# Kernel optimization log

Measured on AMD Instinct MI355X. Metric: run time of the kernel, lower is better.

## Reference

```python
import jax, jax.numpy as jnp
import numpy as np

D_MODEL = 512
NHEAD = 8
HEAD_DIM = D_MODEL // NHEAD
LN_EPS = 1e-5


def layer_norm(x, gamma, beta):
    mu = jnp.mean(x, axis=-1, keepdims=True)
    var = jnp.var(x, axis=-1, keepdims=True)
    return (x - mu) * jax.lax.rsqrt(var + LN_EPS) * gamma + beta


def setup_inputs() -> dict:
    key = jax.random.key(0)
    ks = jax.random.split(key, 10)
    B, L, S = 2, 4096, 4096
    d = D_MODEL
    s = 0.02
    return {
        "x": jax.random.normal(ks[0], (B, L, d), dtype=jnp.float32),
        "source": jax.random.normal(ks[1], (B, S, d), dtype=jnp.float32),
        "Wq": jax.random.normal(ks[2], (d, d), dtype=jnp.float32) * s,
        "Wk": jax.random.normal(ks[3], (d, d), dtype=jnp.float32) * s,
        "Wv": jax.random.normal(ks[4], (d, d), dtype=jnp.float32) * s,
        "Wm": jax.random.normal(ks[5], (d, d), dtype=jnp.float32) * s,
        "W1": jax.random.normal(ks[6], (2 * d, 2 * d), dtype=jnp.float32) * s,
        "W2": jax.random.normal(ks[7], (d, 2 * d), dtype=jnp.float32) * s,
        "g1": jnp.ones((d,), dtype=jnp.float32),
        "b1": jnp.zeros((d,), dtype=jnp.float32),
        "g2": jnp.ones((d,), dtype=jnp.float32),
        "b2": jnp.zeros((d,), dtype=jnp.float32),
    }


def reference(x, source, Wq, Wk, Wv, Wm, W1, W2, g1, b1, g2, b2):
    bs, L, _ = x.shape
    S = source.shape[1]
    # projections (torch Linear: y = x @ W^T), split into heads
    qw = (x @ Wq.T).reshape(bs, L, NHEAD, HEAD_DIM)
    kw = (source @ Wk.T).reshape(bs, S, NHEAD, HEAD_DIM)
    vw = (source @ Wv.T).reshape(bs, S, NHEAD, HEAD_DIM)
    # attention scores [B, L, S, H], softmax over S (axis=2)
    a = jnp.einsum('nlhd,nshd->nlsh', qw, kw) / jnp.sqrt(jnp.float32(HEAD_DIM))
    a = jax.nn.softmax(a, axis=2)
    o = jnp.einsum('nlsh,nshd->nlhd', a, vw).reshape(bs, L, NHEAD * HEAD_DIM)
    message = layer_norm(o @ Wm.T, g1, b1)
    h = jnp.concatenate([x, message], axis=2)  # [B, L, 2D]
    h = jax.nn.relu(h @ W1.T) @ W2.T
    message = layer_norm(h, g2, b2)
    return x + message
```

## Files before the change

kernel.cpp:

```cpp
#include <hip/hip_runtime.h>
#include <stdint.h>

typedef short bh8 __attribute__((ext_vector_type(8)));
typedef float fx4 __attribute__((ext_vector_type(4)));
typedef float fx16 __attribute__((ext_vector_type(16)));
typedef unsigned short u16;
typedef unsigned int u32;
typedef u32 u32x4 __attribute__((ext_vector_type(4)));
typedef u16 us4 __attribute__((ext_vector_type(4)));

#define NHEAD 8
#define HD 64
#define DM 512
#define SEQ 4096
#define ROWS 8192
#define CEXP 0.1803368801111244f

#define MODE_F32 0
#define MODE_BF16 1
#define MODE_RELU_BF16 2
#define MODE_KV 3

__device__ __forceinline__ u16 f2bf(float f) {
  union { float f; u32 u; } x; x.f = f;
  u32 u = x.u;
  u = u + 0x7fffu + ((u >> 16) & 1u);
  return (u16)(u >> 16);
}
__device__ __forceinline__ float bf2f(u16 h) {
  union { u32 u; float f; } x; x.u = ((u32)h) << 16;
  return x.f;
}
__device__ __forceinline__ void gll16(const void* g, void* l) {
  __builtin_amdgcn_global_load_lds(
      (const __attribute__((address_space(1))) void*)(uintptr_t)g,
      (__attribute__((address_space(3))) void*)(uintptr_t)l,
      16, 0, 0);
}
__device__ __forceinline__ fx4 mfma16(bh8 a, bh8 b, fx4 c) {
  return __builtin_amdgcn_mfma_f32_16x16x32_bf16(a, b, c, 0, 0, 0);
}
__device__ __forceinline__ fx16 mfma32(bh8 a, bh8 b, fx16 c) {
  return __builtin_amdgcn_mfma_f32_32x32x16_bf16(a, b, c, 0, 0, 0);
}
__device__ __forceinline__ u32 cvtpk(float lo, float hi) {
  u32 r; asm("v_cvt_pk_bf16_f32 %0, %1, %2" : "=v"(r) : "v"(lo), "v"(hi));
  return r;
}
__device__ __forceinline__ void pswap(u32& a, u32& b) {
  auto r = __builtin_amdgcn_permlane32_swap(a, b, false, false);
  a = r[0]; b = r[1];
}

__global__ __launch_bounds__(256) void cvt_all_kernel(
    const float* __restrict__ x, const float* __restrict__ src,
    const float* __restrict__ Wq, const float* __restrict__ Wk,
    const float* __restrict__ Wv, const float* __restrict__ Wm,
    const float* __restrict__ W1, const float* __restrict__ W2,
    u16* __restrict__ xb, u16* __restrict__ sb,
    u16* __restrict__ wqb, u16* __restrict__ wkvb, u16* __restrict__ wmb,
    u16* __restrict__ w1b, u16* __restrict__ w2b) {
  const int NQ = ROWS * DM / 4;
  const int TOT = 2 * NQ + 655360;
  for (int i = blockIdx.x * 256 + threadIdx.x; i < TOT; i += gridDim.x * 256) {
    const float* s; u16* d; int j;
    if (i < NQ)            { s = x;  d = xb;  j = i; }
    else if (i < 2 * NQ)   { s = src; d = sb; j = i - NQ; }
    else {
      int k = i - 2 * NQ;
      if (k < 65536)       { s = Wq; d = wqb;           j = k; }
      else if (k < 131072) { s = Wk; d = wkvb;          j = k - 65536; }
      else if (k < 196608) { s = Wv; d = wkvb + 262144; j = k - 131072; }
      else if (k < 262144) { s = Wm; d = wmb;           j = k - 196608; }
      else if (k < 524288) { s = W1; d = w1b;           j = k - 262144; }
      else                 { s = W2; d = w2b;           j = k - 524288; }
    }
    float4 v = ((const float4*)s)[j];
    us4 o; o.x = f2bf(v.x); o.y = f2bf(v.y); o.z = f2bf(v.z); o.w = f2bf(v.w);
    ((us4*)d)[j] = o;
  }
}

__device__ __forceinline__ void gemm_body(
    char* smem, const u16* __restrict__ A, const u16* __restrict__ Bw,
    void* __restrict__ Cp, void* __restrict__ C2p,
    int N, int K, int mode, float scl, int bx, int by) {
  char* sA = smem;
  char* sB = smem + 128 * 128;
  const int tid = threadIdx.x;
  const int w = tid >> 6, l = tid & 63;
  const int fr = l & 15, fg = l >> 4;
  const int row0 = by * 128, col0 = bx * 128;
  const int wr = (w >> 1) * 64, wc = (w & 1) * 64;

  fx4 acc[4][4];
#pragma unroll
  for (int m = 0; m < 4; m++)
#pragma unroll
    for (int n = 0; n < 4; n++)
#pragma unroll
      for (int r = 0; r < 4; r++) acc[m][n][r] = 0.f;

  for (int k0 = 0; k0 < K; k0 += 64) {
    __syncthreads();
#pragma unroll
    for (int i = 0; i < 4; i++) {
      int t = i * 256 + tid;
      int r = t >> 3, g = t & 7;
      int gs = g ^ (r & 7);
      gll16(A + (size_t)(row0 + r) * K + k0 + gs * 8, sA + i * 4096 + w * 1024);
      gll16(Bw + (size_t)(col0 + r) * K + k0 + gs * 8, sB + i * 4096 + w * 1024);
    }
    __syncthreads();
#pragma unroll
    for (int ks = 0; ks < 2; ks++) {
      bh8 af[4], bfr[4];
#pragma unroll
      for (int m = 0; m < 4; m++) {
        int rr = wr + m * 16 + fr;
        af[m] = *(const bh8*)(sA + rr * 128 + ((ks * 64 + fg * 16) ^ ((rr & 7) << 4)));
      }
#pragma unroll
      for (int n = 0; n < 4; n++) {
        int rr = wc + n * 16 + fr;
        bfr[n] = *(const bh8*)(sB + rr * 128 + ((ks * 64 + fg * 16) ^ ((rr & 7) << 4)));
      }
      __builtin_amdgcn_s_setprio(1);
#pragma unroll
      for (int m = 0; m < 4; m++)
#pragma unroll
        for (int n = 0; n < 4; n++) acc[m][n] = mfma16(af[m], bfr[n], acc[m][n]);
      __builtin_amdgcn_s_setprio(0);
    }
  }
#pragma unroll
  for (int m = 0; m < 4; m++)
#pragma unroll
    for (int n = 0; n < 4; n++)
#pragma unroll
      for (int r = 0; r < 4; r++) {
        int row = row0 + wr + m * 16 + fg * 4 + r;
        int col = col0 + wc + n * 16 + fr;
        float v = acc[m][n][r];
        if (mode == MODE_F32) {
          ((float*)Cp)[(size_t)row * N + col] = v;
        } else if (mode == MODE_BF16) {
          ((u16*)Cp)[(size_t)row * N + col] = f2bf(v * scl);
        } else if (mode == MODE_RELU_BF16) {
          ((u16*)Cp)[(size_t)row * N + col] = f2bf(v > 0.f ? v : 0.f);
        } else {
          int bb = row >> 12, s = row & 4095;
          if (col < 512) {
            int h = col >> 6, dd = col & 63;
            ((u16*)Cp)[(((size_t)((bb * 8 + h) * 8 + (dd >> 3))) * SEQ + s) * 8 + (dd & 7)] = f2bf(v);
          } else {
            int dd2 = col - 512;
            int h = dd2 >> 6, dd = dd2 & 63;
            ((u16*)C2p)[(((size_t)((bb * 8 + h) * 512 + (s >> 3))) * 64 + dd) * 8 + (s & 7)] = f2bf(v);
          }
        }
      }
}

__global__ __launch_bounds__(256) void qkv_kernel(
    const u16* __restrict__ xb, const u16* __restrict__ sb,
    const u16* __restrict__ wqb, const u16* __restrict__ wkvb,
    u16* __restrict__ Qb, u16* __restrict__ K2, u16* __restrict__ V2) {
  __shared__ __attribute__((aligned(16))) char smem[2 * 128 * 128];
  int bid = blockIdx.x;
  if (bid < 256) {
    gemm_body(smem, xb, wqb, Qb, nullptr, 512, 512, MODE_BF16, CEXP, bid & 3, bid >> 2);
  } else {
    int kb = bid - 256;
    gemm_body(smem, sb, wkvb, K2, V2, 1024, 512, MODE_KV, 1.0f, kb & 7, kb >> 3);
  }
}

__global__ __launch_bounds__(256) void gemm_bt_kernel(
    const u16* __restrict__ A, const u16* __restrict__ Bw,
    void* __restrict__ Cp, int N, int K, int mode) {
  __shared__ __attribute__((aligned(16))) char smem[2 * 128 * 128];
  gemm_body(smem, A, Bw, Cp, nullptr, N, K, mode, 1.0f, blockIdx.x, blockIdx.y);
}

__global__ __launch_bounds__(256) void gemm64_kernel(
    const u16* __restrict__ A, const u16* __restrict__ Bw,
    void* __restrict__ Cp, int M, int N, int K, int mode, float scl) {
  __shared__ __attribute__((aligned(16))) char smem[128 * 128 + 64 * 128];
  char* sA = smem;
  char* sB = smem + 128 * 128;
  const int tid = threadIdx.x;
  const int w = tid >> 6, l = tid & 63;
  const int fr = l & 15, fg = l >> 4;
  const int row0 = blockIdx.y * 128, col0 = blockIdx.x * 64;
  const int wr = (w >> 1) * 64, wc = (w & 1) * 32;

  fx4 acc[4][2];
#pragma unroll
  for (int m = 0; m < 4; m++)
#pragma unroll
    for (int n = 0; n < 2; n++)
#pragma unroll
      for (int r = 0; r < 4; r++) acc[m][n][r] = 0.f;

  for (int k0 = 0; k0 < K; k0 += 64) {
    __syncthreads();
#pragma unroll
    for (int i = 0; i < 4; i++) {
      int t = i * 256 + tid;
      int r = t >> 3, g = t & 7;
      int gs = g ^ (r & 7);
      gll16(A + (size_t)(row0 + r) * K + k0 + gs * 8, sA + i * 4096 + w * 1024);
    }
#pragma unroll
    for (int i = 0; i < 2; i++) {
      int t = i * 256 + tid;
      int r = t >> 3, g = t & 7;
      int gs = g ^ (r & 7);
      gll16(Bw + (size_t)(col0 + r) * K + k0 + gs * 8, sB + i * 4096 + w * 1024);
    }
    __syncthreads();
#pragma unroll
    for (int ks = 0; ks < 2; ks++) {
      bh8 af[4], bfr[2];
#pragma unroll
      for (int m = 0; m < 4; m++) {
        int rr = wr + m * 16 + fr;
        af[m] = *(const bh8*)(sA + rr * 128 + ((ks * 64 + fg * 16) ^ ((rr & 7) << 4)));
      }
#pragma unroll
      for (int n = 0; n < 2; n++) {
        int rr = wc + n * 16 + fr;
        bfr[n] = *(const bh8*)(sB + rr * 128 + ((ks * 64 + fg * 16) ^ ((rr & 7) << 4)));
      }
      __builtin_amdgcn_s_setprio(1);
#pragma unroll
      for (int m = 0; m < 4; m++)
#pragma unroll
        for (int n = 0; n < 2; n++) acc[m][n] = mfma16(af[m], bfr[n], acc[m][n]);
      __builtin_amdgcn_s_setprio(0);
    }
  }
#pragma unroll
  for (int m = 0; m < 4; m++)
#pragma unroll
    for (int n = 0; n < 2; n++)
#pragma unroll
      for (int r = 0; r < 4; r++) {
        int row = row0 + wr + m * 16 + fg * 4 + r;
        int col = col0 + wc + n * 16 + fr;
        float v = acc[m][n][r];
        if (mode == MODE_F32) ((float*)Cp)[(size_t)row * N + col] = v;
        else                  ((u16*)Cp)[(size_t)row * N + col] = f2bf(v * scl);
      }
}

__global__ __launch_bounds__(256, 3) void attn_kernel(
    const u16* __restrict__ Q, const u16* __restrict__ K2,
    const u16* __restrict__ V2,
    u16* __restrict__ Op0, u16* __restrict__ Op1,
    u16* __restrict__ Op2, u16* __restrict__ Op3,
    float* __restrict__ lsum, int ss) {
  const int tid = threadIdx.x;
  const int w = tid >> 6, l = tid & 63;
  const int l31 = l & 31, hi = l >> 5;

  int dl = blockIdx.x;
  int c = dl & 7, j = dl >> 3;
  int bh = 2 * c + (j >> (5 + ss));
  int rest = j & ((32 << ss) - 1);
  int qb = rest & 31, half = rest >> 5;
  const int b = bh >> 3, h = bh & 7;
  const int qr0 = b * SEQ + qb * 128 + w * 32;
  const int chunk = SEQ >> ss;
  const int sbase = half * chunk;
  const int NT = chunk / 64;

  bh8 qf[4];
#pragma unroll
  for (int ks = 0; ks < 4; ks++)
    qf[ks] = *(const bh8*)(Q + (size_t)(qr0 + l31) * DM + h * HD + ks * 16 + hi * 8);

  const u16* Kbase = K2 + (size_t)bh * 8 * SEQ * 8;
  const u16* Vbase = V2 + (size_t)bh * 512 * 64 * 8;

  fx16 o0, o1;
#pragma unroll
  for (int r = 0; r < 16; r++) { o0[r] = 0.f; o1[r] = 0.f; }
  float l_run = 0.f;

  for (int t = 0; t < NT; ++t) {
    const int s0 = sbase + t * 64;

    bh8 kf0[4], kf1[4];
#pragma unroll
    for (int ks = 0; ks < 4; ks++) {
      const u16* kp = Kbase + ((size_t)(ks * 2 + hi) * SEQ + s0 + l31) * 8;
      kf0[ks] = *(const bh8*)kp;
      kf1[ks] = *(const bh8*)(kp + 32 * 8);
    }

    fx16 s0v, s1v;
#pragma unroll
    for (int r = 0; r < 16; r++) { s0v[r] = 0.f; s1v[r] = 0.f; }
    __builtin_amdgcn_s_setprio(1);
#pragma unroll
    for (int ks = 0; ks < 4; ks++) {
      s0v = mfma32(kf0[ks], qf[ks], s0v);
      s1v = mfma32(kf1[ks], qf[ks], s1v);
    }
    __builtin_amdgcn_s_setprio(0);

    bh8 vf0[4], vf1[4];
#pragma unroll
    for (int ks = 0; ks < 4; ks++) {
      const u16* vp = Vbase + ((size_t)((s0 >> 3) + ks * 2 + hi) * 64 + l31) * 8;
      vf0[ks] = *(const bh8*)vp;
      vf1[ks] = *(const bh8*)(vp + 32 * 8);
    }

    float rs = 0.f;
#pragma unroll
    for (int r = 0; r < 16; r++) {
      s0v[r] = __builtin_amdgcn_exp2f(s0v[r]); rs += s0v[r];
    }
#pragma unroll
    for (int r = 0; r < 16; r++) {
      s1v[r] = __builtin_amdgcn_exp2f(s1v[r]); rs += s1v[r];
    }
    l_run += rs;

    __builtin_amdgcn_s_setprio(1);
#pragma unroll
    for (int ks = 0; ks < 4; ks++) {
      int o8 = (ks & 1) * 8;
      u32 w0a, w1a, w0b, w1b;
      if (ks < 2) {
        w0a = cvtpk(s0v[o8 + 0], s0v[o8 + 1]);
        w1a = cvtpk(s0v[o8 + 2], s0v[o8 + 3]);
        w0b = cvtpk(s0v[o8 + 4], s0v[o8 + 5]);
        w1b = cvtpk(s0v[o8 + 6], s0v[o8 + 7]);
      } else {
        w0a = cvtpk(s1v[o8 + 0], s1v[o8 + 1]);
        w1a = cvtpk(s1v[o8 + 2], s1v[o8 + 3]);
        w0b = cvtpk(s1v[o8 + 4], s1v[o8 + 5]);
        w1b = cvtpk(s1v[o8 + 6], s1v[o8 + 7]);
      }
      pswap(w0a, w0b); pswap(w1a, w1b);
      u32x4 fw; fw.x = w0a; fw.y = w1a; fw.z = w0b; fw.w = w1b;
      bh8 pa = __builtin_bit_cast(bh8, fw);
      o0 = mfma32(pa, vf0[ks], o0);
      o1 = mfma32(pa, vf1[ks], o1);
    }
    __builtin_amdgcn_s_setprio(0);
  }

  l_run += __shfl_xor(l_run, 32);
  if (hi == 0)
    lsum[half * 65536 + bh * 4096 + ((qr0 & 4095) + l31)] = l_run;
  u16* Op = (half == 0) ? Op0 : (half == 1) ? Op1 : (half == 2) ? Op2 : Op3;
#pragma unroll
  for (int r = 0; r < 16; r++) {
    int crow = (r & 3) + 8 * (r >> 2) + 4 * hi;
    size_t row = (size_t)(qr0 + crow);
    Op[row * DM + h * HD + l31] = f2bf(o0[r]);
    Op[row * DM + h * HD + 32 + l31] = f2bf(o1[r]);
  }
}

__global__ __launch_bounds__(256) void merge_kernel(
    const u16* __restrict__ Oa, const u16* __restrict__ Ob,
    const u16* __restrict__ Oc, const u16* __restrict__ Od,
    const float* __restrict__ lsum, u16* __restrict__ out, int split) {
  int i8 = blockIdx.x * 256 + threadIdx.x;
  size_t base = (size_t)i8 * 8;
  if (base >= (size_t)ROWS * DM) return;
  int row = (int)(base >> 9), col = (int)(base & 511);
  int h = col >> 6, b = row >> 12, lr = row & 4095;
  int li = (b * 8 + h) * 4096 + lr;
  float acc[8];
#pragma unroll
  for (int j = 0; j < 8; j++) acc[j] = 0.f;
  float lt = 0.f;
  const u16* ops[4] = {Oa, Ob, Oc, Od};
  for (int s = 0; s < split; s++) {
    lt += lsum[s * 65536 + li];
    bh8 v = *(const bh8*)(ops[s] + base);
#pragma unroll
    for (int j = 0; j < 8; j++) acc[j] += bf2f((u16)v[j]);
  }
  float inv = 1.f / lt;
  bh8 o;
#pragma unroll
  for (int j = 0; j < 8; j++) o[j] = (short)f2bf(acc[j] * inv);
  *(bh8*)(out + base) = o;
}

__global__ __launch_bounds__(256) void ln_concat_kernel(
    const u16* __restrict__ M0, const u16* __restrict__ xb,
    const float* __restrict__ g1, const float* __restrict__ b1,
    u16* __restrict__ h) {
  const int row = blockIdx.x;
  const int tid = threadIdx.x;
  const u16* mr = M0 + (size_t)row * 512;
  float v0 = bf2f(mr[tid]), v1 = bf2f(mr[tid + 256]);
  float s = v0 + v1, s2 = v0 * v0 + v1 * v1;
#pragma unroll
  for (int off = 1; off <= 32; off <<= 1) {
    s += __shfl_xor(s, off);
    s2 += __shfl_xor(s2, off);
  }
  __shared__ float red[8];
  const int w = tid >> 6, l = tid & 63;
  if (l == 0) { red[w] = s; red[w + 4] = s2; }
  __syncthreads();
  s = red[0] + red[1] + red[2] + red[3];
  s2 = red[4] + red[5] + red[6] + red[7];
  float mu = s * (1.f / 512.f);
  float var = s2 * (1.f / 512.f) - mu * mu;
  float rstd = rsqrtf(var + 1e-5f);
  u16* hr = h + (size_t)row * 1024;
  const u16* xrow = xb + (size_t)row * 512;
  for (int e = tid; e < 512; e += 256) {
    hr[e] = xrow[e];
    hr[512 + e] = f2bf((bf2f(mr[e]) - mu) * rstd * g1[e] + b1[e]);
  }
}

__global__ __launch_bounds__(256) void ln_res_kernel(
    const float* __restrict__ F, const float* __restrict__ X,
    const float* __restrict__ g2, const float* __restrict__ b2,
    float* __restrict__ out) {
  const int row = blockIdx.x;
  const int tid = threadIdx.x;
  const float* fr_ = F + (size_t)row * 512;
  float v0 = fr_[tid], v1 = fr_[tid + 256];
  float s = v0 + v1, s2 = v0 * v0 + v1 * v1;
#pragma unroll
  for (int off = 1; off <= 32; off <<= 1) {
    s += __shfl_xor(s, off);
    s2 += __shfl_xor(s2, off);
  }
  __shared__ float red[8];
  const int w = tid >> 6, l = tid & 63;
  if (l == 0) { red[w] = s; red[w + 4] = s2; }
  __syncthreads();
  s = red[0] + red[1] + red[2] + red[3];
  s2 = red[4] + red[5] + red[6] + red[7];
  float mu = s * (1.f / 512.f);
  float var = s2 * (1.f / 512.f) - mu * mu;
  float rstd = rsqrtf(var + 1e-5f);
  const float* xr = X + (size_t)row * 512;
  float* orow = out + (size_t)row * 512;
  for (int e = tid; e < 512; e += 256)
    orow[e] = xr[e] + (fr_[e] - mu) * rstd * g2[e] + b2[e];
}

extern "C" void kernel_launch(void* const* d_in, const int* in_sizes, int n_in,
                              void* d_out, int out_size, void* d_ws, size_t ws_size,
                              hipStream_t stream) {
  (void)in_sizes; (void)n_in; (void)out_size;
  const float* x   = (const float*)d_in[0];
  const float* src = (const float*)d_in[1];
  const float* Wq  = (const float*)d_in[2];
  const float* Wk  = (const float*)d_in[3];
  const float* Wv  = (const float*)d_in[4];
  const float* Wm  = (const float*)d_in[5];
  const float* W1  = (const float*)d_in[6];
  const float* W2  = (const float*)d_in[7];
  const float* g1  = (const float*)d_in[8];
  const float* b1  = (const float*)d_in[9];
  const float* g2  = (const float*)d_in[10];
  const float* b2  = (const float*)d_in[11];

  char* ws = (char*)d_ws;
  u16* xb   = (u16*)(ws + 0);
  u16* sb   = (u16*)(ws + 8388608);
  u16* wqb  = (u16*)(ws + 16777216);
  u16* wkvb = (u16*)(ws + 17301504);
  u16* wmb  = (u16*)(ws + 18350080);
  u16* w1b  = (u16*)(ws + 18874368);
  u16* w2b  = (u16*)(ws + 20971520);
  u16* Qb   = (u16*)(ws + 22020096);
  u16* K2b  = (u16*)(ws + 30408704);
  u16* V2b  = (u16*)(ws + 38797312);
  u16* Op0  = (u16*)(ws + 47185920);
  u16* Op1  = (u16*)(ws + 8388608);

  const bool big = ws_size >= 73400320u;
  int ss = big ? 2 : 1;
  u16* Op2; u16* Op3; float* lsum;
  if (big) {
    Op2  = (u16*)(ws + 55574528);
    Op3  = (u16*)(ws + 63963136);
    lsum = (float*)(ws + 72351744);
  } else {
    Op2  = Op0; Op3 = Op0;
    lsum = (float*)(ws + 55574528);
  }
  u16* Obf  = (u16*)(ws + 22020096);
  u16* M0b  = (u16*)(ws + 30408704);
  u16* hb   = (u16*)(ws + 38797312);
  u16* h1b  = (u16*)(ws + 22020096);
  float* fb = (float*)(ws + 38797312);

  cvt_all_kernel<<<2048, 256, 0, stream>>>(x, src, Wq, Wk, Wv, Wm, W1, W2,
                                           xb, sb, wqb, wkvb, wmb, w1b, w2b);
  qkv_kernel<<<768, 256, 0, stream>>>(xb, sb, wqb, wkvb, Qb, K2b, V2b);
  attn_kernel<<<512 << ss, 256, 0, stream>>>(Qb, K2b, V2b, Op0, Op1, Op2, Op3, lsum, ss);
  merge_kernel<<<2048, 256, 0, stream>>>(Op0, Op1, Op2, Op3, lsum, Obf, 1 << ss);
  gemm64_kernel<<<dim3(8, 64), 256, 0, stream>>>(Obf, wmb, M0b, ROWS, 512, 512, MODE_BF16, 1.0f);
  ln_concat_kernel<<<8192, 256, 0, stream>>>(M0b, xb, g1, b1, hb);
  gemm_bt_kernel<<<dim3(8, 64), 256, 0, stream>>>(hb, w1b, h1b, 1024, 1024, MODE_RELU_BF16);
  gemm64_kernel<<<dim3(8, 64), 256, 0, stream>>>(h1b, w2b, fb, ROWS, 512, 1024, MODE_F32, 1.0f);
  ln_res_kernel<<<8192, 256, 0, stream>>>(fb, x, g2, b2, (float*)d_out);
}
```

Baseline: 224.6 us.

## Pre-swizzle weights into MFMA fragment order and load B directly to registers

Weights are converted into an MFMA-fragment-ordered layout during the bf16 conversion pass, so the GEMM core loads B fragments straight from global memory into registers and no longer stages B through LDS. The FFN1 GEMM reads its A operand from two separate sources (x and the normalized message), which removes the concat copy in the layernorm kernel. The FFN2 output is now stored as bf16 instead of f32, halving its write and read traffic at some cost in precision. The trade-off is uncoalesced-looking direct global B loads that depend on cache hits, plus halved LDS use.

```diff
diff --git a/kernel.cpp b/kernel.cpp
--- a/kernel.cpp
+++ b/kernel.cpp
@@ -16,7 +16,6 @@
 #define ROWS 8192
 #define CEXP 0.1803368801111244f
 
-#define MODE_F32 0
 #define MODE_BF16 1
 #define MODE_RELU_BF16 2
 #define MODE_KV 3
@@ -50,6 +49,11 @@
 __device__ __forceinline__ void pswap(u32& a, u32& b) {
   auto r = __builtin_amdgcn_permlane32_swap(a, b, false, false);
   a = r[0]; b = r[1];
+}
+
+__device__ __forceinline__ int fragidx4(int n, int k4, int K) {
+  return (((((n >> 4) * (K >> 5) + (k4 >> 5)) << 2) + ((k4 >> 3) & 3)) * 16 + (n & 15)) * 2
+         + ((k4 & 7) >> 2);
 }
 
 __global__ __launch_bounds__(256) void cvt_all_kernel(
@@ -63,88 +67,93 @@
   const int NQ = ROWS * DM / 4;
   const int TOT = 2 * NQ + 655360;
   for (int i = blockIdx.x * 256 + threadIdx.x; i < TOT; i += gridDim.x * 256) {
-    const float* s; u16* d; int j;
+    const float* s; u16* d; int j; int widx = -1;
     if (i < NQ)            { s = x;  d = xb;  j = i; }
     else if (i < 2 * NQ)   { s = src; d = sb; j = i - NQ; }
     else {
       int k = i - 2 * NQ;
-      if (k < 65536)       { s = Wq; d = wqb;           j = k; }
-      else if (k < 131072) { s = Wk; d = wkvb;          j = k - 65536; }
-      else if (k < 196608) { s = Wv; d = wkvb + 262144; j = k - 131072; }
-      else if (k < 262144) { s = Wm; d = wmb;           j = k - 196608; }
-      else if (k < 524288) { s = W1; d = w1b;           j = k - 262144; }
-      else                 { s = W2; d = w2b;           j = k - 524288; }
+      int n, k4, K;
+      if (k < 65536)       { s = Wq; d = wqb; j = k;          n = j >> 7; k4 = (j & 127) << 2; K = 512; }
+      else if (k < 131072) { s = Wk; d = wkvb; j = k - 65536; n = j >> 7; k4 = (j & 127) << 2; K = 512; }
+      else if (k < 196608) { s = Wv; d = wkvb; j = k - 131072; n = (j >> 7) + 512; k4 = (j & 127) << 2; K = 512; }
+      else if (k < 262144) { s = Wm; d = wmb; j = k - 196608; n = j >> 7; k4 = (j & 127) << 2; K = 512; }
+      else if (k < 524288) { s = W1; d = w1b; j = k - 262144; n = j >> 8; k4 = (j & 255) << 2; K = 1024; }
+      else                 { s = W2; d = w2b; j = k - 524288; n = j >> 8; k4 = (j & 255) << 2; K = 1024; }
+      widx = fragidx4(n, k4, K);
     }
     float4 v = ((const float4*)s)[j];
     us4 o; o.x = f2bf(v.x); o.y = f2bf(v.y); o.z = f2bf(v.z); o.w = f2bf(v.w);
-    ((us4*)d)[j] = o;
-  }
-}
-
-__device__ __forceinline__ void gemm_body(
-    char* smem, const u16* __restrict__ A, const u16* __restrict__ Bw,
-    void* __restrict__ Cp, void* __restrict__ C2p,
+    ((us4*)d)[widx < 0 ? j : widx] = o;
+  }
+}
+
+template <int NTW>
+__device__ __forceinline__ void gemm_core(
+    char* sA, const u16* __restrict__ A, const u16* __restrict__ A2, int strideA,
+    const u16* __restrict__ Bw, void* __restrict__ Cp, void* __restrict__ C2p,
     int N, int K, int mode, float scl, int bx, int by) {
-  char* sA = smem;
-  char* sB = smem + 128 * 128;
   const int tid = threadIdx.x;
   const int w = tid >> 6, l = tid & 63;
   const int fr = l & 15, fg = l >> 4;
-  const int row0 = by * 128, col0 = bx * 128;
-  const int wr = (w >> 1) * 64, wc = (w & 1) * 64;
-
-  fx4 acc[4][4];
+  const int row0 = by * 128, col0 = bx * NTW * 32;
+  const int wr = (w >> 1) * 64, wc = (w & 1) * NTW * 16;
+
+  fx4 acc[4][NTW];
 #pragma unroll
   for (int m = 0; m < 4; m++)
 #pragma unroll
-    for (int n = 0; n < 4; n++)
+    for (int n = 0; n < NTW; n++)
 #pragma unroll
       for (int r = 0; r < 4; r++) acc[m][n][r] = 0.f;
 
   for (int k0 = 0; k0 < K; k0 += 64) {
+    const u16* Asrc = (k0 < 512) ? A : A2;
+    const int kk = k0 & (strideA - 1);
     __syncthreads();
 #pragma unroll
     for (int i = 0; i < 4; i++) {
       int t = i * 256 + tid;
       int r = t >> 3, g = t & 7;
       int gs = g ^ (r & 7);
-      gll16(A + (size_t)(row0 + r) * K + k0 + gs * 8, sA + i * 4096 + w * 1024);
-      gll16(Bw + (size_t)(col0 + r) * K + k0 + gs * 8, sB + i * 4096 + w * 1024);
-    }
+      gll16(Asrc + (size_t)(row0 + r) * strideA + kk + gs * 8, sA + i * 4096 + w * 1024);
+    }
+    bh8 bfr[2][NTW];
+#pragma unroll
+    for (int ks = 0; ks < 2; ks++)
+#pragma unroll
+      for (int n = 0; n < NTW; n++) {
+        const u16* bp = Bw +
+            ((((size_t)((col0 + wc) >> 4) + n) * (K >> 5) + (k0 >> 5) + ks) * 4 + fg) * 128 +
+            fr * 8;
+        bfr[ks][n] = *(const bh8*)bp;
+      }
     __syncthreads();
 #pragma unroll
     for (int ks = 0; ks < 2; ks++) {
-      bh8 af[4], bfr[4];
+      bh8 af[4];
 #pragma unroll
       for (int m = 0; m < 4; m++) {
         int rr = wr + m * 16 + fr;
         af[m] = *(const bh8*)(sA + rr * 128 + ((ks * 64 + fg * 16) ^ ((rr & 7) << 4)));
       }
-#pragma unroll
-      for (int n = 0; n < 4; n++) {
-        int rr = wc + n * 16 + fr;
-        bfr[n] = *(const bh8*)(sB + rr * 128 + ((ks * 64 + fg * 16) ^ ((rr & 7) << 4)));
-      }
       __builtin_amdgcn_s_setprio(1);
 #pragma unroll
       for (int m = 0; m < 4; m++)
 #pragma unroll
-        for (int n = 0; n < 4; n++) acc[m][n] = mfma16(af[m], bfr[n], acc[m][n]);
+        for (int n = 0; n < NTW; n++) acc[m][n] = mfma16(af[m], bfr[ks][n], acc[m][n]);
       __builtin_amdgcn_s_setprio(0);
     }
   }
 #pragma unroll
   for (int m = 0; m < 4; m++)
 #pragma unroll
-    for (int n = 0; n < 4; n++)
+    for (int n = 0; n < NTW; n++)
 #pragma unroll
       for (int r = 0; r < 4; r++) {
         int row = row0 + wr + m * 16 + fg * 4 + r;
         int col = col0 + wc + n * 16 + fr;
         float v = acc[m][n][r];
-        if (mode == MODE_F32) {
-          ((float*)Cp)[(size_t)row * N + col] = v;
-        } else if (mode == MODE_BF16) {
+        if (mode == MODE_BF16) {
           ((u16*)Cp)[(size_t)row * N + col] = f2bf(v * scl);
         } else if (mode == MODE_RELU_BF16) {
           ((u16*)Cp)[(size_t)row * N + col] = f2bf(v > 0.f ? v : 0.f);
@@ -166,93 +175,32 @@
     const u16* __restrict__ xb, const u16* __restrict__ sb,
     const u16* __restrict__ wqb, const u16* __restrict__ wkvb,
     u16* __restrict__ Qb, u16* __restrict__ K2, u16* __restrict__ V2) {
-  __shared__ __attribute__((aligned(16))) char smem[2 * 128 * 128];
+  __shared__ __attribute__((aligned(16))) char smem[128 * 128];
   int bid = blockIdx.x;
   if (bid < 256) {
-    gemm_body(smem, xb, wqb, Qb, nullptr, 512, 512, MODE_BF16, CEXP, bid & 3, bid >> 2);
+    gemm_core<4>(smem, xb, xb, 512, wqb, Qb, nullptr, 512, 512, MODE_BF16, CEXP,
+                 bid & 3, bid >> 2);
   } else {
     int kb = bid - 256;
-    gemm_body(smem, sb, wkvb, K2, V2, 1024, 512, MODE_KV, 1.0f, kb & 7, kb >> 3);
-  }
-}
-
-__global__ __launch_bounds__(256) void gemm_bt_kernel(
-    const u16* __restrict__ A, const u16* __restrict__ Bw,
-    void* __restrict__ Cp, int N, int K, int mode) {
-  __shared__ __attribute__((aligned(16))) char smem[2 * 128 * 128];
-  gemm_body(smem, A, Bw, Cp, nullptr, N, K, mode, 1.0f, blockIdx.x, blockIdx.y);
+    gemm_core<4>(smem, sb, sb, 512, wkvb, K2, V2, 1024, 512, MODE_KV, 1.0f,
+                 kb & 7, kb >> 3);
+  }
+}
+
+__global__ __launch_bounds__(256) void ffn1_kernel(
+    const u16* __restrict__ xb, const u16* __restrict__ m0ln,
+    const u16* __restrict__ w1b, u16* __restrict__ h1) {
+  __shared__ __attribute__((aligned(16))) char smem[128 * 128];
+  gemm_core<4>(smem, xb, m0ln, 512, w1b, h1, nullptr, 1024, 1024, MODE_RELU_BF16, 1.0f,
+               blockIdx.x, blockIdx.y);
 }
 
 __global__ __launch_bounds__(256) void gemm64_kernel(
-    const u16* __restrict__ A, const u16* __restrict__ Bw,
-    void* __restrict__ Cp, int M, int N, int K, int mode, float scl) {
-  __shared__ __attribute__((aligned(16))) char smem[128 * 128 + 64 * 128];
-  char* sA = smem;
-  char* sB = smem + 128 * 128;
-  const int tid = threadIdx.x;
-  const int w = tid >> 6, l = tid & 63;
-  const int fr = l & 15, fg = l >> 4;
-  const int row0 = blockIdx.y * 128, col0 = blockIdx.x * 64;
-  const int wr = (w >> 1) * 64, wc = (w & 1) * 32;
-
-  fx4 acc[4][2];
-#pragma unroll
-  for (int m = 0; m < 4; m++)
-#pragma unroll
-    for (int n = 0; n < 2; n++)
-#pragma unroll
-      for (int r = 0; r < 4; r++) acc[m][n][r] = 0.f;
-
-  for (int k0 = 0; k0 < K; k0 += 64) {
-    __syncthreads();
-#pragma unroll
-    for (int i = 0; i < 4; i++) {
-      int t = i * 256 + tid;
-      int r = t >> 3, g = t & 7;
-      int gs = g ^ (r & 7);
-      gll16(A + (size_t)(row0 + r) * K + k0 + gs * 8, sA + i * 4096 + w * 1024);
-    }
-#pragma unroll
-    for (int i = 0; i < 2; i++) {
-      int t = i * 256 + tid;
-      int r = t >> 3, g = t & 7;
-      int gs = g ^ (r & 7);
-      gll16(Bw + (size_t)(col0 + r) * K + k0 + gs * 8, sB + i * 4096 + w * 1024);
-    }
-    __syncthreads();
-#pragma unroll
-    for (int ks = 0; ks < 2; ks++) {
-      bh8 af[4], bfr[2];
-#pragma unroll
-      for (int m = 0; m < 4; m++) {
-        int rr = wr + m * 16 + fr;
-        af[m] = *(const bh8*)(sA + rr * 128 + ((ks * 64 + fg * 16) ^ ((rr & 7) << 4)));
-      }
-#pragma unroll
-      for (int n = 0; n < 2; n++) {
-        int rr = wc + n * 16 + fr;
-        bfr[n] = *(const bh8*)(sB + rr * 128 + ((ks * 64 + fg * 16) ^ ((rr & 7) << 4)));
-      }
-      __builtin_amdgcn_s_setprio(1);
-#pragma unroll
-      for (int m = 0; m < 4; m++)
-#pragma unroll
-        for (int n = 0; n < 2; n++) acc[m][n] = mfma16(af[m], bfr[n], acc[m][n]);
-      __builtin_amdgcn_s_setprio(0);
-    }
-  }
-#pragma unroll
-  for (int m = 0; m < 4; m++)
-#pragma unroll
-    for (int n = 0; n < 2; n++)
-#pragma unroll
-      for (int r = 0; r < 4; r++) {
-        int row = row0 + wr + m * 16 + fg * 4 + r;
-        int col = col0 + wc + n * 16 + fr;
-        float v = acc[m][n][r];
-        if (mode == MODE_F32) ((float*)Cp)[(size_t)row * N + col] = v;
-        else                  ((u16*)Cp)[(size_t)row * N + col] = f2bf(v * scl);
-      }
+    const u16* __restrict__ A, const u16* __restrict__ A2, int strideA,
+    const u16* __restrict__ Bw, u16* __restrict__ Cp, int K, float scl) {
+  __shared__ __attribute__((aligned(16))) char smem[128 * 128];
+  gemm_core<2>(smem, A, A2, strideA, Bw, Cp, nullptr, 512, K, MODE_BF16, scl,
+               blockIdx.x, blockIdx.y);
 }
 
 __global__ __launch_bounds__(256, 3) void attn_kernel(
@@ -396,10 +344,9 @@
   *(bh8*)(out + base) = o;
 }
 
-__global__ __launch_bounds__(256) void ln_concat_kernel(
-    const u16* __restrict__ M0, const u16* __restrict__ xb,
-    const float* __restrict__ g1, const float* __restrict__ b1,
-    u16* __restrict__ h) {
+__global__ __launch_bounds__(256) void ln_kernel(
+    const u16* __restrict__ M0, const float* __restrict__ g1,
+    const float* __restrict__ b1, u16* __restrict__ out) {
   const int row = blockIdx.x;
   const int tid = threadIdx.x;
   const u16* mr = M0 + (size_t)row * 512;
@@ -419,22 +366,19 @@
   float mu = s * (1.f / 512.f);
   float var = s2 * (1.f / 512.f) - mu * mu;
   float rstd = rsqrtf(var + 1e-5f);
-  u16* hr = h + (size_t)row * 1024;
-  const u16* xrow = xb + (size_t)row * 512;
-  for (int e = tid; e < 512; e += 256) {
-    hr[e] = xrow[e];
-    hr[512 + e] = f2bf((bf2f(mr[e]) - mu) * rstd * g1[e] + b1[e]);
-  }
+  u16* orow = out + (size_t)row * 512;
+  for (int e = tid; e < 512; e += 256)
+    orow[e] = f2bf((bf2f(mr[e]) - mu) * rstd * g1[e] + b1[e]);
 }
 
 __global__ __launch_bounds__(256) void ln_res_kernel(
-    const float* __restrict__ F, const float* __restrict__ X,
+    const u16* __restrict__ F, const float* __restrict__ X,
     const float* __restrict__ g2, const float* __restrict__ b2,
     float* __restrict__ out) {
   const int row = blockIdx.x;
   const int tid = threadIdx.x;
-  const float* fr_ = F + (size_t)row * 512;
-  float v0 = fr_[tid], v1 = fr_[tid + 256];
+  const u16* fr_ = F + (size_t)row * 512;
+  float v0 = bf2f(fr_[tid]), v1 = bf2f(fr_[tid + 256]);
   float s = v0 + v1, s2 = v0 * v0 + v1 * v1;
 #pragma unroll
   for (int off = 1; off <= 32; off <<= 1) {
@@ -453,7 +397,7 @@
   const float* xr = X + (size_t)row * 512;
   float* orow = out + (size_t)row * 512;
   for (int e = tid; e < 512; e += 256)
-    orow[e] = xr[e] + (fr_[e] - mu) * rstd * g2[e] + b2[e];
+    orow[e] = xr[e] + (bf2f(fr_[e]) - mu) * rstd * g2[e] + b2[e];
 }
 
 extern "C" void kernel_launch(void* const* d_in, const int* in_sizes, int n_in,
@@ -500,18 +444,18 @@
   }
   u16* Obf  = (u16*)(ws + 22020096);
   u16* M0b  = (u16*)(ws + 30408704);
-  u16* hb   = (u16*)(ws + 38797312);
+  u16* m0ln = (u16*)(ws + 38797312);
   u16* h1b  = (u16*)(ws + 22020096);
-  float* fb = (float*)(ws + 38797312);
+  u16* fb   = (u16*)(ws + 47185920);
 
   cvt_all_kernel<<<2048, 256, 0, stream>>>(x, src, Wq, Wk, Wv, Wm, W1, W2,
                                            xb, sb, wqb, wkvb, wmb, w1b, w2b);
   qkv_kernel<<<768, 256, 0, stream>>>(xb, sb, wqb, wkvb, Qb, K2b, V2b);
   attn_kernel<<<512 << ss, 256, 0, stream>>>(Qb, K2b, V2b, Op0, Op1, Op2, Op3, lsum, ss);
   merge_kernel<<<2048, 256, 0, stream>>>(Op0, Op1, Op2, Op3, lsum, Obf, 1 << ss);
-  gemm64_kernel<<<dim3(8, 64), 256, 0, stream>>>(Obf, wmb, M0b, ROWS, 512, 512, MODE_BF16, 1.0f);
-  ln_concat_kernel<<<8192, 256, 0, stream>>>(M0b, xb, g1, b1, hb);
-  gemm_bt_kernel<<<dim3(8, 64), 256, 0, stream>>>(hb, w1b, h1b, 1024, 1024, MODE_RELU_BF16);
-  gemm64_kernel<<<dim3(8, 64), 256, 0, stream>>>(h1b, w2b, fb, ROWS, 512, 1024, MODE_F32, 1.0f);
+  gemm64_kernel<<<dim3(8, 64), 256, 0, stream>>>(Obf, Obf, 512, wmb, M0b, 512, 1.0f);
+  ln_kernel<<<8192, 256, 0, stream>>>(M0b, g1, b1, m0ln);
+  ffn1_kernel<<<dim3(8, 64), 256, 0, stream>>>(xb, m0ln, w1b, h1b);
+  gemm64_kernel<<<dim3(8, 64), 256, 0, stream>>>(h1b, h1b, 1024, w2b, fb, 1024, 1.0f);
   ln_res_kernel<<<8192, 256, 0, stream>>>(fb, x, g2, b2, (float*)d_out);
 }
```

Measured after the change: 221.3 us. About the same (-1.5%).
